# Kernel tuning notes

Measured on AMD Instinct MI355X. Metric: run time of the kernel, lower is better.

## Reference

```python
import jax, jax.numpy as jnp
import numpy as np

N = 8  # nodes per sample (hardcoded in preprocess)
NEG_SLOPE = 0.2
BIG_NEG = -1e30


def _mlp3(x, w1, b1, w2, b2, w3, b3):
    h = jax.nn.relu(x @ w1 + b1)
    h = jax.nn.relu(h @ w2 + b2)
    return h @ w3 + b3


def _gabriel(p):
    # p: [B,N,3] (vis_latent). Returns symmetric boolean adjacency [B,N,N]
    # (no self loops) and pairwise distances [B,N,N].
    mid = (p[:, :, None, :] + p[:, None, :, :]) * 0.5          # [B,N,N,3]
    r2 = jnp.sum((p[:, :, None, :] - mid) ** 2, axis=-1)       # [B,N,N]
    # d2[b,i,j,k] = ||p[b,k] - mid[b,i,j]||^2
    d2 = jnp.sum((p[:, None, None, :, :] - mid[:, :, :, None, :]) ** 2, axis=-1)  # [B,N,N,N]
    eye = jnp.eye(N, dtype=bool)
    kmask = (~eye[:, None, :]) & (~eye[None, :, :])            # [N,N,N] k != i, k != j
    viol = jnp.any(kmask[None] & (d2 < r2[..., None]), axis=-1)
    adj = (~viol) & (~eye)[None]                               # [B,N,N]
    dist = jnp.sqrt(jnp.sum((p[:, :, None, :] - p[:, None, :, :]) ** 2, axis=-1) + 1e-30)
    return adj, dist


def _gatv2(x, mask, eattr, wl, bl, wr, br, we, att, bias):
    # Dense masked GATv2 (PyG semantics, heads=1).
    # x: [B,N,F]; mask: [B,N,N] bool (row i = target, col j = source);
    # eattr: [B,N,N,1] edge feature.
    xl = x @ wl + bl                                            # source transform [B,N,C]
    xr = x @ wr + br                                            # target transform [B,N,C]
    ee = eattr @ we                                             # [B,N,N,C]
    h = xr[:, :, None, :] + xl[:, None, :, :] + ee              # [B,N,N,C]
    h = jnp.where(h >= 0, h, NEG_SLOPE * h)                     # leaky_relu
    e = jnp.einsum('bijc,c->bij', h, att)
    e = jnp.where(mask, e, BIG_NEG)
    alpha = jax.nn.softmax(e, axis=-1) * mask                   # rows always contain self loop
    return jnp.einsum('bij,bjc->bic', alpha, xl) + bias


def _forward(x, enc_w1, enc_b1, enc_w2, enc_b2, enc_w3, enc_b3,
             g1_wl, g1_bl, g1_wr, g1_br, g1_we, g1_att, g1_bias,
             g2_wl, g2_bl, g2_wr, g2_br, g2_we, g2_att, g2_bias,
             skip_w, skip_b, dec_w1, dec_b1, dec_w2, dec_b2, dec_w3, dec_b3):
    B = x.shape[0]
    # preprocess: [agent_type=0, index, value]
    idx = jnp.broadcast_to(jnp.arange(N, dtype=x.dtype), (B, N))
    xp = jnp.stack([jnp.zeros_like(x), idx, x], axis=-1)        # [B,N,3]

    latent = _mlp3(xp, enc_w1, enc_b1, enc_w2, enc_b2, enc_w3, enc_b3)  # [B,N,3]
    vis = latent - jnp.mean(latent, axis=1, keepdims=True)
    std = jnp.std(vis, axis=1, ddof=1) + 1e-8                   # torch.std is unbiased
    vis = vis / std[:, None, :]

    adj, dist = _gabriel(vis)                                   # [B,N,N] bool / float
    eye = jnp.eye(N, dtype=bool)[None]
    mask = adj | eye                                            # add self loops
    n_edges = jnp.sum(adj, axis=(1, 2)).astype(x.dtype)
    mean_attr = jnp.sum(dist * adj, axis=(1, 2)) / jnp.maximum(n_edges, 1.0)
    eattr = jnp.where(eye, mean_attr[:, None, None], dist)[..., None]  # [B,N,N,1]

    h1 = jax.nn.relu(_gatv2(latent, mask, eattr, g1_wl, g1_bl, g1_wr, g1_br, g1_we, g1_att, g1_bias))
    h2 = _gatv2(h1, mask, eattr, g2_wl, g2_bl, g2_wr, g2_br, g2_we, g2_att, g2_bias)
    combined = h2 + latent @ skip_w + skip_b
    rec = _mlp3(combined, dec_w1, dec_b1, dec_w2, dec_b2, dec_w3, dec_b3)
    return xp, rec, vis, adj


def setup_inputs() -> dict:
    key = jax.random.key(0)
    ks = iter(jax.random.split(key, 32))
    B, H, L, F = 16384, 64, 3, 3

    def rn(shape, scale):
        return (jax.random.normal(next(ks), shape, dtype=jnp.float32) * scale)

    inp = {
        'x': jax.random.normal(next(ks), (B, N), dtype=jnp.float32),
        'enc_w1': rn((F, H), (1.0 / F) ** 0.5), 'enc_b1': jnp.zeros((H,), jnp.float32),
        'enc_w2': rn((H, H), (1.0 / H) ** 0.5), 'enc_b2': jnp.zeros((H,), jnp.float32),
        'enc_w3': rn((H, L), (1.0 / H) ** 0.5), 'enc_b3': jnp.zeros((L,), jnp.float32),
        'g1_wl': rn((L, H), (1.0 / L) ** 0.5), 'g1_bl': jnp.zeros((H,), jnp.float32),
        'g1_wr': rn((L, H), (1.0 / L) ** 0.5), 'g1_br': jnp.zeros((H,), jnp.float32),
        'g1_we': rn((1, H), 1.0), 'g1_att': rn((H,), (1.0 / H) ** 0.5),
        'g1_bias': jnp.zeros((H,), jnp.float32),
        'g2_wl': rn((H, L), (1.0 / H) ** 0.5), 'g2_bl': jnp.zeros((L,), jnp.float32),
        'g2_wr': rn((H, L), (1.0 / H) ** 0.5), 'g2_br': jnp.zeros((L,), jnp.float32),
        'g2_we': rn((1, L), 1.0), 'g2_att': rn((L,), (1.0 / L) ** 0.5),
        'g2_bias': jnp.zeros((L,), jnp.float32),
        'skip_w': rn((L, L), (1.0 / L) ** 0.5), 'skip_b': jnp.zeros((L,), jnp.float32),
        'dec_w1': rn((L, H), (1.0 / L) ** 0.5), 'dec_b1': jnp.zeros((H,), jnp.float32),
        'dec_w2': rn((H, H), (1.0 / H) ** 0.5), 'dec_b2': jnp.zeros((H,), jnp.float32),
        'dec_w3': rn((H, F), (1.0 / H) ** 0.5), 'dec_b3': jnp.zeros((F,), jnp.float32),
    }
    return inp


def reference(x, enc_w1, enc_b1, enc_w2, enc_b2, enc_w3, enc_b3,
              g1_wl, g1_bl, g1_wr, g1_br, g1_we, g1_att, g1_bias,
              g2_wl, g2_bl, g2_wr, g2_br, g2_we, g2_att, g2_bias,
              skip_w, skip_b, dec_w1, dec_b1, dec_w2, dec_b2, dec_w3, dec_b3):
    return _forward(x, enc_w1, enc_b1, enc_w2, enc_b2, enc_w3, enc_b3,
                    g1_wl, g1_bl, g1_wr, g1_br, g1_we, g1_att, g1_bias,
                    g2_wl, g2_bl, g2_wr, g2_br, g2_we, g2_att, g2_bias,
                    skip_w, skip_b, dec_w1, dec_b1, dec_w2, dec_b2, dec_w3, dec_b3)
```

## Files before the change

kernel.cpp:

```cpp
#include <hip/hip_runtime.h>
#include <math.h>


#define WFENCE() asm volatile("s_waitcnt lgkmcnt(0)" ::: "memory")

struct alignas(16) WaveScratch {
  union Big {
    double d[8][68];
    float  f[2][8][68];
  } big;
  float  alphaS[64];
  float  latSf[24];
  float  xl2S[24];
  float  xr2S[24];
  float  combS[24];
  double latSd[24];
  double visSd[24];
};

__global__ __launch_bounds__(256)
void gae_fused(const float* __restrict__ x,
               const float* __restrict__ enc_w1, const float* __restrict__ enc_b1,
               const float* __restrict__ enc_w2, const float* __restrict__ enc_b2,
               const float* __restrict__ enc_w3, const float* __restrict__ enc_b3,
               const float* __restrict__ g1_wl, const float* __restrict__ g1_bl,
               const float* __restrict__ g1_wr, const float* __restrict__ g1_br,
               const float* __restrict__ g1_we, const float* __restrict__ g1_att,
               const float* __restrict__ g1_bias,
               const float* __restrict__ g2_wl, const float* __restrict__ g2_bl,
               const float* __restrict__ g2_wr, const float* __restrict__ g2_br,
               const float* __restrict__ g2_we, const float* __restrict__ g2_att,
               const float* __restrict__ g2_bias,
               const float* __restrict__ skip_w, const float* __restrict__ skip_b,
               const float* __restrict__ dec_w1, const float* __restrict__ dec_b1,
               const float* __restrict__ dec_w2, const float* __restrict__ dec_b2,
               const float* __restrict__ dec_w3, const float* __restrict__ dec_b3,
               float* __restrict__ out, int B)
{
  __shared__ WaveScratch ws4[4];
  __shared__ __align__(16) float s_w3e[192];
  __shared__ __align__(16) float s_w3d[192];
  __shared__ __align__(16) float s_g2wl[192];
  __shared__ __align__(16) float s_g2wr[192];
  __shared__ __align__(16) float s_we1[64];
  __shared__ __align__(16) float s_att1[64];
  __shared__ float s_skw[9], s_skb[3], s_b3e[3], s_b3d[3];
  __shared__ float s_g2bl[3], s_g2br[3], s_g2we[3], s_g2att[3], s_g2bias[3];

  const int tid  = threadIdx.x;
  const int wid  = tid >> 6;
  const int lane = tid & 63;

  if (tid < 192) { s_w3e[tid] = enc_w3[tid]; s_w3d[tid] = dec_w3[tid];
                   s_g2wl[tid] = g2_wl[tid]; s_g2wr[tid] = g2_wr[tid]; }
  if (tid < 64)  { s_we1[tid] = g1_we[tid];  s_att1[tid] = g1_att[tid]; }
  if (tid < 9)   s_skw[tid] = skip_w[tid];
  if (tid < 3)   { s_skb[tid] = skip_b[tid]; s_b3e[tid] = enc_b3[tid]; s_b3d[tid] = dec_b3[tid];
                   s_g2bl[tid] = g2_bl[tid]; s_g2br[tid] = g2_br[tid]; s_g2we[tid] = g2_we[tid];
                   s_g2att[tid] = g2_att[tid]; s_g2bias[tid] = g2_bias[tid]; }

  const int s = blockIdx.x * 4 + wid;
  const bool active = (s < B);
  const int sc = active ? s : 0;
  WaveScratch& W = ws4[wid];

  const double ew1n = (double)enc_w1[64 + lane];
  const double ew1x = (double)enc_w1[128 + lane];
  const double eb1d = (double)enc_b1[lane];
  const double eb2d = (double)enc_b2[lane];
  const float wl0 = g1_wl[lane], wl1 = g1_wl[64 + lane], wl2 = g1_wl[128 + lane], blc = g1_bl[lane];
  const float wr0 = g1_wr[lane], wr1 = g1_wr[64 + lane], wr2 = g1_wr[128 + lane], brc = g1_br[lane];
  const float g1bias_c = g1_bias[lane];
  const float dwc0 = dec_w1[lane], dwc1 = dec_w1[64 + lane], dwc2 = dec_w1[128 + lane];
  const float db1c = dec_b1[lane], db2c = dec_b2[lane];

  __syncthreads();

  const float* xb = x + (size_t)sc * 8;
  if (active && lane < 24) {
    const int r = lane, n = r / 3, l = r - n * 3;
    float v = (l == 0) ? 0.0f : ((l == 1) ? (float)n : xb[n]);
    out[(size_t)s * 24 + r] = v;
  }
  #pragma unroll
  for (int n = 0; n < 8; ++n) {
    double v = (double)n * ew1n + (double)xb[n] * ew1x + eb1d;
    W.big.d[n][lane] = v > 0.0 ? v : 0.0;
  }
  WFENCE();

  double acc2[8];
  #pragma unroll
  for (int n = 0; n < 8; ++n) acc2[n] = eb2d;
  #pragma unroll
  for (int ch = 0; ch < 4; ++ch) {
    double wcd[16];
    #pragma unroll
    for (int t = 0; t < 16; ++t) wcd[t] = (double)enc_w2[(ch * 16 + t) * 64 + lane];
    #pragma unroll
    for (int t2 = 0; t2 < 8; ++t2) {
      #pragma unroll
      for (int n = 0; n < 8; ++n) {
        const double2 hv = *(const double2*)&W.big.d[n][ch * 16 + t2 * 2];
        acc2[n] = fma(hv.x, wcd[t2 * 2], acc2[n]);
        acc2[n] = fma(hv.y, wcd[t2 * 2 + 1], acc2[n]);
      }
    }
  }
  WFENCE();
  #pragma unroll
  for (int n = 0; n < 8; ++n) W.big.d[n][lane] = acc2[n] > 0.0 ? acc2[n] : 0.0;
  WFENCE();

  {
    const int r24 = lane & 31, g = lane >> 5;
    double a = 0.0;
    if (r24 < 24) {
      const int n = r24 / 3, l = r24 - n * 3;
      a = g ? 0.0 : (double)s_b3e[l];
      const int k0 = g * 32;
      #pragma unroll 8
      for (int k = k0; k < k0 + 32; ++k) a = fma(W.big.d[n][k], (double)s_w3e[k * 3 + l], a);
    }
    const double b = __shfl_xor(a, 32);
    if (lane < 24) {
      const double tot = a + b;
      W.latSd[lane] = tot;
      W.latSf[lane] = (float)tot;
    }
  }
  WFENCE();

  if (lane < 24) {
    const int r = lane, l = r % 3;
    double s1 = 0.0;
    #pragma unroll
    for (int q = 0; q < 8; ++q) s1 += W.latSd[q * 3 + l];
    const double m = s1 * 0.125;
    double s2 = 0.0;
    #pragma unroll
    for (int q = 0; q < 8; ++q) s2 += (W.latSd[q * 3 + l] - m);
    const double m2 = s2 * 0.125;
    double s3 = 0.0;
    #pragma unroll
    for (int q = 0; q < 8; ++q) { double dv = W.latSd[q * 3 + l] - m - m2; s3 += dv * dv; }
    const double stdv = sqrt(s3 / 7.0) + 1e-8;
    const double visv = (W.latSd[r] - m) / stdv;
    W.visSd[r] = visv;
    if (active) out[(size_t)B * 48 + (size_t)s * 24 + r] = (float)visv;
  }
  WFENCE();

  const int gi = lane >> 3, gj = lane & 7;
  const double pi0 = W.visSd[gi * 3], pi1 = W.visSd[gi * 3 + 1], pi2 = W.visSd[gi * 3 + 2];
  const double pj0 = W.visSd[gj * 3], pj1 = W.visSd[gj * 3 + 1], pj2 = W.visSd[gj * 3 + 2];
  const double mid0 = (pi0 + pj0) * 0.5, mid1 = (pi1 + pj1) * 0.5, mid2 = (pi2 + pj2) * 0.5;
  const double dr0 = pi0 - mid0, dr1 = pi1 - mid1, dr2 = pi2 - mid2;
  const double r2 = dr0 * dr0 + dr1 * dr1 + dr2 * dr2;
  bool viol = false;
  #pragma unroll
  for (int k = 0; k < 8; ++k) {
    const double a0 = W.visSd[k * 3] - mid0;
    const double a1 = W.visSd[k * 3 + 1] - mid1;
    const double a2 = W.visSd[k * 3 + 2] - mid2;
    const double d2 = a0 * a0 + a1 * a1 + a2 * a2;
    viol = viol || ((k != gi) && (k != gj) && (d2 < r2));
  }
  const double dd0 = pi0 - pj0, dd1 = pi1 - pj1, dd2 = pi2 - pj2;
  const double distd = sqrt(dd0 * dd0 + dd1 * dd1 + dd2 * dd2 + 1e-30);
  const bool adjb  = (!viol) && (gi != gj);
  const bool maskb = adjb || (gi == gj);
  const float adjf = adjb ? 1.0f : 0.0f;
  if (active) out[(size_t)B * 72 + (size_t)s * 64 + lane] = adjf;
  const float distf = (float)distd;
  float ne = adjf, sd = adjb ? distf : 0.0f;
  #pragma unroll
  for (int d = 1; d < 64; d <<= 1) { ne += __shfl_xor(ne, d); sd += __shfl_xor(sd, d); }
  const float mean_attr = sd / fmaxf(ne, 1.0f);
  const float eat = (gi == gj) ? mean_attr : distf;

  float xlr[8], xrr[8];
  #pragma unroll
  for (int n = 0; n < 8; ++n) {
    const float a0 = W.latSf[n * 3], a1 = W.latSf[n * 3 + 1], a2 = W.latSf[n * 3 + 2];
    xlr[n] = fmaf(a2, wl2, fmaf(a1, wl1, fmaf(a0, wl0, blc)));
    xrr[n] = fmaf(a2, wr2, fmaf(a1, wr1, fmaf(a0, wr0, brc)));
    W.big.f[0][n][lane] = xlr[n];
    W.big.f[1][n][lane] = xrr[n];
  }
  WFENCE();

  float ev = 0.0f;
  #pragma unroll
  for (int c4 = 0; c4 < 16; ++c4) {
    const float4 xlv = *(const float4*)&W.big.f[0][gj][c4 * 4];
    const float4 xrv = *(const float4*)&W.big.f[1][gi][c4 * 4];
    const float4 wev = *(const float4*)&s_we1[c4 * 4];
    const float4 atv = *(const float4*)&s_att1[c4 * 4];
    float h;
    h = fmaf(eat, wev.x, xrv.x + xlv.x); ev = fmaf(fmaxf(h, 0.f) + 0.2f * fminf(h, 0.f), atv.x, ev);
    h = fmaf(eat, wev.y, xrv.y + xlv.y); ev = fmaf(fmaxf(h, 0.f) + 0.2f * fminf(h, 0.f), atv.y, ev);
    h = fmaf(eat, wev.z, xrv.z + xlv.z); ev = fmaf(fmaxf(h, 0.f) + 0.2f * fminf(h, 0.f), atv.z, ev);
    h = fmaf(eat, wev.w, xrv.w + xlv.w); ev = fmaf(fmaxf(h, 0.f) + 0.2f * fminf(h, 0.f), atv.w, ev);
  }
  {
    float em = maskb ? ev : -1e30f;
    float mx = em;
    mx = fmaxf(mx, __shfl_xor(mx, 1)); mx = fmaxf(mx, __shfl_xor(mx, 2)); mx = fmaxf(mx, __shfl_xor(mx, 4));
    float p = __expf(em - mx);
    float ssum = p;
    ssum += __shfl_xor(ssum, 1); ssum += __shfl_xor(ssum, 2); ssum += __shfl_xor(ssum, 4);
    W.alphaS[lane] = (p / ssum) * (maskb ? 1.0f : 0.0f);
  }
  WFENCE();

  float hg[8];
  #pragma unroll
  for (int i = 0; i < 8; ++i) {
    const float4 q0 = *(const float4*)&W.alphaS[i * 8];
    const float4 q1 = *(const float4*)&W.alphaS[i * 8 + 4];
    float a = g1bias_c;
    a = fmaf(q0.x, xlr[0], a); a = fmaf(q0.y, xlr[1], a);
    a = fmaf(q0.z, xlr[2], a); a = fmaf(q0.w, xlr[3], a);
    a = fmaf(q1.x, xlr[4], a); a = fmaf(q1.y, xlr[5], a);
    a = fmaf(q1.z, xlr[6], a); a = fmaf(q1.w, xlr[7], a);
    hg[i] = fmaxf(a, 0.0f);
  }
  WFENCE();
  #pragma unroll
  for (int i = 0; i < 8; ++i) W.big.f[0][i][lane] = hg[i];
  WFENCE();

  if (lane < 48) {
    const int g = lane / 24, r = lane - g * 24, n = r / 3, l = r - n * 3;
    const float* wsel = g ? s_g2wr : s_g2wl;
    float a = g ? s_g2br[l] : s_g2bl[l];
    #pragma unroll 8
    for (int k = 0; k < 64; ++k) a = fmaf(W.big.f[0][n][k], wsel[k * 3 + l], a);
    if (g) W.xr2S[r] = a; else W.xl2S[r] = a;
  }
  WFENCE();

  float e2 = 0.0f;
  #pragma unroll
  for (int l = 0; l < 3; ++l) {
    const float hh = fmaf(eat, s_g2we[l], W.xr2S[gi * 3 + l] + W.xl2S[gj * 3 + l]);
    e2 = fmaf(fmaxf(hh, 0.f) + 0.2f * fminf(hh, 0.f), s_g2att[l], e2);
  }
  {
    float em = maskb ? e2 : -1e30f;
    float mx = em;
    mx = fmaxf(mx, __shfl_xor(mx, 1)); mx = fmaxf(mx, __shfl_xor(mx, 2)); mx = fmaxf(mx, __shfl_xor(mx, 4));
    float p = __expf(em - mx);
    float ssum = p;
    ssum += __shfl_xor(ssum, 1); ssum += __shfl_xor(ssum, 2); ssum += __shfl_xor(ssum, 4);
    W.alphaS[lane] = (p / ssum) * (maskb ? 1.0f : 0.0f);
  }
  WFENCE();

  if (lane < 24) {
    const int r = lane, n = r / 3, l = r - n * 3;
    float a = s_g2bias[l];
    #pragma unroll
    for (int j = 0; j < 8; ++j) a = fmaf(W.alphaS[n * 8 + j], W.xl2S[j * 3 + l], a);
    const float cb = a + W.latSf[n * 3] * s_skw[l] + W.latSf[n * 3 + 1] * s_skw[3 + l]
                       + W.latSf[n * 3 + 2] * s_skw[6 + l] + s_skb[l];
    W.combS[r] = cb;
  }
  WFENCE();

  #pragma unroll
  for (int n = 0; n < 8; ++n) {
    const float c0 = W.combS[n * 3], c1 = W.combS[n * 3 + 1], c2 = W.combS[n * 3 + 2];
    const float d1 = fmaf(c2, dwc2, fmaf(c1, dwc1, fmaf(c0, dwc0, db1c)));
    W.big.f[0][n][lane] = fmaxf(d1, 0.0f);
  }
  WFENCE();

  float accf[8];
  #pragma unroll
  for (int n = 0; n < 8; ++n) accf[n] = db2c;
  #pragma unroll
  for (int ch = 0; ch < 2; ++ch) {
    float wc[32];
    #pragma unroll
    for (int t = 0; t < 32; ++t) wc[t] = dec_w2[(ch * 32 + t) * 64 + lane];
    #pragma unroll
    for (int t4 = 0; t4 < 8; ++t4) {
      #pragma unroll
      for (int n = 0; n < 8; ++n) {
        const float4 hv = *(const float4*)&W.big.f[0][n][ch * 32 + t4 * 4];
        accf[n] = fmaf(hv.x, wc[t4 * 4], accf[n]);
        accf[n] = fmaf(hv.y, wc[t4 * 4 + 1], accf[n]);
        accf[n] = fmaf(hv.z, wc[t4 * 4 + 2], accf[n]);
        accf[n] = fmaf(hv.w, wc[t4 * 4 + 3], accf[n]);
      }
    }
  }
  WFENCE();
  #pragma unroll
  for (int n = 0; n < 8; ++n) W.big.f[1][n][lane] = fmaxf(accf[n], 0.0f);
  WFENCE();

  {
    const int r24 = lane & 31, g = lane >> 5;
    float a = 0.0f;
    if (r24 < 24) {
      const int n = r24 / 3, l = r24 - n * 3;
      a = g ? 0.0f : s_b3d[l];
      const int k0 = g * 32;
      #pragma unroll 8
      for (int k = k0; k < k0 + 32; ++k) a = fmaf(W.big.f[1][n][k], s_w3d[k * 3 + l], a);
    }
    const float b = __shfl_xor(a, 32);
    if (active && lane < 24) {
      out[(size_t)B * 24 + (size_t)s * 24 + lane] = a + b;
    }
  }
}

extern "C" void kernel_launch(void* const* d_in, const int* in_sizes, int n_in,
                              void* d_out, int out_size, void* d_ws, size_t ws_size,
                              hipStream_t stream) {
  const int B = in_sizes[0] / 8;
  const float* x       = (const float*)d_in[0];
  const float* enc_w1  = (const float*)d_in[1];
  const float* enc_b1  = (const float*)d_in[2];
  const float* enc_w2  = (const float*)d_in[3];
  const float* enc_b2  = (const float*)d_in[4];
  const float* enc_w3  = (const float*)d_in[5];
  const float* enc_b3  = (const float*)d_in[6];
  const float* g1_wl   = (const float*)d_in[7];
  const float* g1_bl   = (const float*)d_in[8];
  const float* g1_wr   = (const float*)d_in[9];
  const float* g1_br   = (const float*)d_in[10];
  const float* g1_we   = (const float*)d_in[11];
  const float* g1_att  = (const float*)d_in[12];
  const float* g1_bias = (const float*)d_in[13];
  const float* g2_wl   = (const float*)d_in[14];
  const float* g2_bl   = (const float*)d_in[15];
  const float* g2_wr   = (const float*)d_in[16];
  const float* g2_br   = (const float*)d_in[17];
  const float* g2_we   = (const float*)d_in[18];
  const float* g2_att  = (const float*)d_in[19];
  const float* g2_bias = (const float*)d_in[20];
  const float* skip_w  = (const float*)d_in[21];
  const float* skip_b  = (const float*)d_in[22];
  const float* dec_w1  = (const float*)d_in[23];
  const float* dec_b1  = (const float*)d_in[24];
  const float* dec_w2  = (const float*)d_in[25];
  const float* dec_b2  = (const float*)d_in[26];
  const float* dec_w3  = (const float*)d_in[27];
  const float* dec_b3  = (const float*)d_in[28];
  float* out = (float*)d_out;

  const int nblk = (B + 3) / 4;
  gae_fused<<<nblk, 256, 0, stream>>>(x,
      enc_w1, enc_b1, enc_w2, enc_b2, enc_w3, enc_b3,
      g1_wl, g1_bl, g1_wr, g1_br, g1_we, g1_att, g1_bias,
      g2_wl, g2_bl, g2_wr, g2_br, g2_we, g2_att, g2_bias,
      skip_w, skip_b, dec_w1, dec_b1, dec_w2, dec_b2, dec_w3, dec_b3,
      out, B);
}
```

Baseline: 95.40 us.

## Shrink LDS scratch, cap registers for 8 waves, split accumulators in dot products

Cuts per-wave LDS by overlaying scratch buffers inside the big union and dropping the shared copies of small weight matrices, which are now read straight from global/L2. Launch bounds now request 8 blocks per CU, and the weight-chunk register arrays are halved so more waves fit. Long serial FMA chains are split into four partial accumulators for more ILP, and the mean/std stage uses wave shuffles instead of an LDS round trip. The cost is more global loads of the small weights and possible register spilling under the tighter bound.

```diff
diff --git a/kernel.cpp b/kernel.cpp
--- a/kernel.cpp
+++ b/kernel.cpp
@@ -5,20 +5,15 @@
 #define WFENCE() asm volatile("s_waitcnt lgkmcnt(0)" ::: "memory")
 
 struct alignas(16) WaveScratch {
-  union Big {
+  union {
     double d[8][68];
-    float  f[2][8][68];
+    float  f[16][68];
   } big;
-  float  alphaS[64];
-  float  latSf[24];
-  float  xl2S[24];
-  float  xr2S[24];
-  float  combS[24];
-  double latSd[24];
-  double visSd[24];
+  float extra[112];
+  float latSf[24];
 };
 
-__global__ __launch_bounds__(256)
+__global__ __launch_bounds__(256, 8)
 void gae_fused(const float* __restrict__ x,
                const float* __restrict__ enc_w1, const float* __restrict__ enc_b1,
                const float* __restrict__ enc_w2, const float* __restrict__ enc_b2,
@@ -38,10 +33,6 @@
                float* __restrict__ out, int B)
 {
   __shared__ WaveScratch ws4[4];
-  __shared__ __align__(16) float s_w3e[192];
-  __shared__ __align__(16) float s_w3d[192];
-  __shared__ __align__(16) float s_g2wl[192];
-  __shared__ __align__(16) float s_g2wr[192];
   __shared__ __align__(16) float s_we1[64];
   __shared__ __align__(16) float s_att1[64];
   __shared__ float s_skw[9], s_skb[3], s_b3e[3], s_b3d[3];
@@ -51,8 +42,6 @@
   const int wid  = tid >> 6;
   const int lane = tid & 63;
 
-  if (tid < 192) { s_w3e[tid] = enc_w3[tid]; s_w3d[tid] = dec_w3[tid];
-                   s_g2wl[tid] = g2_wl[tid]; s_g2wr[tid] = g2_wr[tid]; }
   if (tid < 64)  { s_we1[tid] = g1_we[tid];  s_att1[tid] = g1_att[tid]; }
   if (tid < 9)   s_skw[tid] = skip_w[tid];
   if (tid < 3)   { s_skb[tid] = skip_b[tid]; s_b3e[tid] = enc_b3[tid]; s_b3d[tid] = dec_b3[tid];
@@ -93,15 +82,15 @@
   #pragma unroll
   for (int n = 0; n < 8; ++n) acc2[n] = eb2d;
   #pragma unroll
-  for (int ch = 0; ch < 4; ++ch) {
-    double wcd[16];
-    #pragma unroll
-    for (int t = 0; t < 16; ++t) wcd[t] = (double)enc_w2[(ch * 16 + t) * 64 + lane];
-    #pragma unroll
-    for (int t2 = 0; t2 < 8; ++t2) {
+  for (int ch = 0; ch < 8; ++ch) {
+    double wcd[8];
+    #pragma unroll
+    for (int t = 0; t < 8; ++t) wcd[t] = (double)enc_w2[(ch * 8 + t) * 64 + lane];
+    #pragma unroll
+    for (int t2 = 0; t2 < 4; ++t2) {
       #pragma unroll
       for (int n = 0; n < 8; ++n) {
-        const double2 hv = *(const double2*)&W.big.d[n][ch * 16 + t2 * 2];
+        const double2 hv = *(const double2*)&W.big.d[n][ch * 8 + t2 * 2];
         acc2[n] = fma(hv.x, wcd[t2 * 2], acc2[n]);
         acc2[n] = fma(hv.y, wcd[t2 * 2 + 1], acc2[n]);
       }
@@ -112,57 +101,61 @@
   for (int n = 0; n < 8; ++n) W.big.d[n][lane] = acc2[n] > 0.0 ? acc2[n] : 0.0;
   WFENCE();
 
+  double totd;
   {
     const int r24 = lane & 31, g = lane >> 5;
-    double a = 0.0;
-    if (r24 < 24) {
-      const int n = r24 / 3, l = r24 - n * 3;
-      a = g ? 0.0 : (double)s_b3e[l];
-      const int k0 = g * 32;
-      #pragma unroll 8
-      for (int k = k0; k < k0 + 32; ++k) a = fma(W.big.d[n][k], (double)s_w3e[k * 3 + l], a);
-    }
-    const double b = __shfl_xor(a, 32);
+    const int n = (r24 < 24) ? r24 / 3 : 0;
+    const int l = (r24 < 24) ? r24 % 3 : 0;
+    const int k0 = g * 32;
+    double p0 = 0.0, p1 = 0.0, p2 = 0.0, p3 = 0.0;
+    #pragma unroll
+    for (int kk = 0; kk < 8; ++kk) {
+      p0 = fma(W.big.d[n][k0 + kk],      (double)enc_w3[(k0 + kk) * 3 + l],      p0);
+      p1 = fma(W.big.d[n][k0 + 8 + kk],  (double)enc_w3[(k0 + 8 + kk) * 3 + l],  p1);
+      p2 = fma(W.big.d[n][k0 + 16 + kk], (double)enc_w3[(k0 + 16 + kk) * 3 + l], p2);
+      p3 = fma(W.big.d[n][k0 + 24 + kk], (double)enc_w3[(k0 + 24 + kk) * 3 + l], p3);
+    }
+    double a = ((p0 + p1) + (p2 + p3)) + (g ? 0.0 : (double)s_b3e[l]);
+    totd = a + __shfl_xor(a, 32);
+    if (lane < 24) W.latSf[lane] = (float)totd;
+  }
+
+  double* const visSd = (double*)&W.big.f[15][0];
+  {
+    const int l = lane % 3;
+    double v[8];
+    #pragma unroll
+    for (int q = 0; q < 8; ++q) v[q] = __shfl(totd, q * 3 + l);
     if (lane < 24) {
-      const double tot = a + b;
-      W.latSd[lane] = tot;
-      W.latSf[lane] = (float)tot;
-    }
-  }
-  WFENCE();
-
-  if (lane < 24) {
-    const int r = lane, l = r % 3;
-    double s1 = 0.0;
-    #pragma unroll
-    for (int q = 0; q < 8; ++q) s1 += W.latSd[q * 3 + l];
-    const double m = s1 * 0.125;
-    double s2 = 0.0;
-    #pragma unroll
-    for (int q = 0; q < 8; ++q) s2 += (W.latSd[q * 3 + l] - m);
-    const double m2 = s2 * 0.125;
-    double s3 = 0.0;
-    #pragma unroll
-    for (int q = 0; q < 8; ++q) { double dv = W.latSd[q * 3 + l] - m - m2; s3 += dv * dv; }
-    const double stdv = sqrt(s3 / 7.0) + 1e-8;
-    const double visv = (W.latSd[r] - m) / stdv;
-    W.visSd[r] = visv;
-    if (active) out[(size_t)B * 48 + (size_t)s * 24 + r] = (float)visv;
+      const double s1 = ((v[0] + v[1]) + (v[2] + v[3])) + ((v[4] + v[5]) + (v[6] + v[7]));
+      const double m = s1 * 0.125;
+      double s2 = 0.0;
+      #pragma unroll
+      for (int q = 0; q < 8; ++q) s2 += (v[q] - m);
+      const double m2 = s2 * 0.125;
+      double s3 = 0.0;
+      #pragma unroll
+      for (int q = 0; q < 8; ++q) { const double dv = v[q] - m - m2; s3 += dv * dv; }
+      const double stdv = sqrt(s3 / 7.0) + 1e-8;
+      const double visv = (totd - m) / stdv;
+      visSd[lane] = visv;
+      if (active) out[(size_t)B * 48 + (size_t)s * 24 + lane] = (float)visv;
+    }
   }
   WFENCE();
 
   const int gi = lane >> 3, gj = lane & 7;
-  const double pi0 = W.visSd[gi * 3], pi1 = W.visSd[gi * 3 + 1], pi2 = W.visSd[gi * 3 + 2];
-  const double pj0 = W.visSd[gj * 3], pj1 = W.visSd[gj * 3 + 1], pj2 = W.visSd[gj * 3 + 2];
+  const double pi0 = visSd[gi * 3], pi1 = visSd[gi * 3 + 1], pi2 = visSd[gi * 3 + 2];
+  const double pj0 = visSd[gj * 3], pj1 = visSd[gj * 3 + 1], pj2 = visSd[gj * 3 + 2];
   const double mid0 = (pi0 + pj0) * 0.5, mid1 = (pi1 + pj1) * 0.5, mid2 = (pi2 + pj2) * 0.5;
   const double dr0 = pi0 - mid0, dr1 = pi1 - mid1, dr2 = pi2 - mid2;
   const double r2 = dr0 * dr0 + dr1 * dr1 + dr2 * dr2;
   bool viol = false;
   #pragma unroll
   for (int k = 0; k < 8; ++k) {
-    const double a0 = W.visSd[k * 3] - mid0;
-    const double a1 = W.visSd[k * 3 + 1] - mid1;
-    const double a2 = W.visSd[k * 3 + 2] - mid2;
+    const double a0 = visSd[k * 3] - mid0;
+    const double a1 = visSd[k * 3 + 1] - mid1;
+    const double a2 = visSd[k * 3 + 2] - mid2;
     const double d2 = a0 * a0 + a1 * a1 + a2 * a2;
     viol = viol || ((k != gi) && (k != gj) && (d2 < r2));
   }
@@ -185,40 +178,41 @@
     const float a0 = W.latSf[n * 3], a1 = W.latSf[n * 3 + 1], a2 = W.latSf[n * 3 + 2];
     xlr[n] = fmaf(a2, wl2, fmaf(a1, wl1, fmaf(a0, wl0, blc)));
     xrr[n] = fmaf(a2, wr2, fmaf(a1, wr1, fmaf(a0, wr0, brc)));
-    W.big.f[0][n][lane] = xlr[n];
-    W.big.f[1][n][lane] = xrr[n];
-  }
-  WFENCE();
-
-  float ev = 0.0f;
-  #pragma unroll
-  for (int c4 = 0; c4 < 16; ++c4) {
-    const float4 xlv = *(const float4*)&W.big.f[0][gj][c4 * 4];
-    const float4 xrv = *(const float4*)&W.big.f[1][gi][c4 * 4];
-    const float4 wev = *(const float4*)&s_we1[c4 * 4];
-    const float4 atv = *(const float4*)&s_att1[c4 * 4];
-    float h;
-    h = fmaf(eat, wev.x, xrv.x + xlv.x); ev = fmaf(fmaxf(h, 0.f) + 0.2f * fminf(h, 0.f), atv.x, ev);
-    h = fmaf(eat, wev.y, xrv.y + xlv.y); ev = fmaf(fmaxf(h, 0.f) + 0.2f * fminf(h, 0.f), atv.y, ev);
-    h = fmaf(eat, wev.z, xrv.z + xlv.z); ev = fmaf(fmaxf(h, 0.f) + 0.2f * fminf(h, 0.f), atv.z, ev);
-    h = fmaf(eat, wev.w, xrv.w + xlv.w); ev = fmaf(fmaxf(h, 0.f) + 0.2f * fminf(h, 0.f), atv.w, ev);
-  }
-  {
+    W.big.f[n][lane]     = xlr[n];
+    W.big.f[8 + n][lane] = xrr[n];
+  }
+  WFENCE();
+
+  {
+    float ev0 = 0.0f, ev1 = 0.0f, ev2 = 0.0f, ev3 = 0.0f;
+    #pragma unroll
+    for (int c4 = 0; c4 < 16; ++c4) {
+      const float4 xlv = *(const float4*)&W.big.f[gj][c4 * 4];
+      const float4 xrv = *(const float4*)&W.big.f[8 + gi][c4 * 4];
+      const float4 wev = *(const float4*)&s_we1[c4 * 4];
+      const float4 atv = *(const float4*)&s_att1[c4 * 4];
+      float h;
+      h = fmaf(eat, wev.x, xrv.x + xlv.x); ev0 = fmaf(fmaxf(h, 0.f) + 0.2f * fminf(h, 0.f), atv.x, ev0);
+      h = fmaf(eat, wev.y, xrv.y + xlv.y); ev1 = fmaf(fmaxf(h, 0.f) + 0.2f * fminf(h, 0.f), atv.y, ev1);
+      h = fmaf(eat, wev.z, xrv.z + xlv.z); ev2 = fmaf(fmaxf(h, 0.f) + 0.2f * fminf(h, 0.f), atv.z, ev2);
+      h = fmaf(eat, wev.w, xrv.w + xlv.w); ev3 = fmaf(fmaxf(h, 0.f) + 0.2f * fminf(h, 0.f), atv.w, ev3);
+    }
+    const float ev = (ev0 + ev1) + (ev2 + ev3);
     float em = maskb ? ev : -1e30f;
     float mx = em;
     mx = fmaxf(mx, __shfl_xor(mx, 1)); mx = fmaxf(mx, __shfl_xor(mx, 2)); mx = fmaxf(mx, __shfl_xor(mx, 4));
     float p = __expf(em - mx);
     float ssum = p;
     ssum += __shfl_xor(ssum, 1); ssum += __shfl_xor(ssum, 2); ssum += __shfl_xor(ssum, 4);
-    W.alphaS[lane] = (p / ssum) * (maskb ? 1.0f : 0.0f);
+    W.extra[lane] = (p / ssum) * (maskb ? 1.0f : 0.0f);
   }
   WFENCE();
 
   float hg[8];
   #pragma unroll
   for (int i = 0; i < 8; ++i) {
-    const float4 q0 = *(const float4*)&W.alphaS[i * 8];
-    const float4 q1 = *(const float4*)&W.alphaS[i * 8 + 4];
+    const float4 q0 = *(const float4*)&W.extra[i * 8];
+    const float4 q1 = *(const float4*)&W.extra[i * 8 + 4];
     float a = g1bias_c;
     a = fmaf(q0.x, xlr[0], a); a = fmaf(q0.y, xlr[1], a);
     a = fmaf(q0.z, xlr[2], a); a = fmaf(q0.w, xlr[3], a);
@@ -228,33 +222,39 @@
   }
   WFENCE();
   #pragma unroll
-  for (int i = 0; i < 8; ++i) W.big.f[0][i][lane] = hg[i];
+  for (int i = 0; i < 8; ++i) W.big.f[i][lane] = hg[i];
   WFENCE();
 
   if (lane < 48) {
     const int g = lane / 24, r = lane - g * 24, n = r / 3, l = r - n * 3;
-    const float* wsel = g ? s_g2wr : s_g2wl;
-    float a = g ? s_g2br[l] : s_g2bl[l];
-    #pragma unroll 8
-    for (int k = 0; k < 64; ++k) a = fmaf(W.big.f[0][n][k], wsel[k * 3 + l], a);
-    if (g) W.xr2S[r] = a; else W.xl2S[r] = a;
-  }
-  WFENCE();
-
-  float e2 = 0.0f;
-  #pragma unroll
-  for (int l = 0; l < 3; ++l) {
-    const float hh = fmaf(eat, s_g2we[l], W.xr2S[gi * 3 + l] + W.xl2S[gj * 3 + l]);
-    e2 = fmaf(fmaxf(hh, 0.f) + 0.2f * fminf(hh, 0.f), s_g2att[l], e2);
-  }
-  {
+    const float* __restrict__ wsel = g ? g2_wr : g2_wl;
+    float p0 = 0.f, p1 = 0.f, p2 = 0.f, p3 = 0.f;
+    #pragma unroll
+    for (int kk = 0; kk < 16; ++kk) {
+      p0 = fmaf(W.big.f[n][kk],      wsel[(kk) * 3 + l],      p0);
+      p1 = fmaf(W.big.f[n][16 + kk], wsel[(16 + kk) * 3 + l], p1);
+      p2 = fmaf(W.big.f[n][32 + kk], wsel[(32 + kk) * 3 + l], p2);
+      p3 = fmaf(W.big.f[n][48 + kk], wsel[(48 + kk) * 3 + l], p3);
+    }
+    const float a = ((p0 + p1) + (p2 + p3)) + (g ? s_g2br[l] : s_g2bl[l]);
+    W.extra[64 + g * 24 + r] = a;
+  }
+  WFENCE();
+
+  {
+    float e2 = 0.0f;
+    #pragma unroll
+    for (int l = 0; l < 3; ++l) {
+      const float hh = fmaf(eat, s_g2we[l], W.extra[88 + gi * 3 + l] + W.extra[64 + gj * 3 + l]);
+      e2 = fmaf(fmaxf(hh, 0.f) + 0.2f * fminf(hh, 0.f), s_g2att[l], e2);
+    }
     float em = maskb ? e2 : -1e30f;
     float mx = em;
     mx = fmaxf(mx, __shfl_xor(mx, 1)); mx = fmaxf(mx, __shfl_xor(mx, 2)); mx = fmaxf(mx, __shfl_xor(mx, 4));
     float p = __expf(em - mx);
     float ssum = p;
     ssum += __shfl_xor(ssum, 1); ssum += __shfl_xor(ssum, 2); ssum += __shfl_xor(ssum, 4);
-    W.alphaS[lane] = (p / ssum) * (maskb ? 1.0f : 0.0f);
+    W.extra[lane] = (p / ssum) * (maskb ? 1.0f : 0.0f);
   }
   WFENCE();
 
@@ -262,18 +262,21 @@
     const int r = lane, n = r / 3, l = r - n * 3;
     float a = s_g2bias[l];
     #pragma unroll
-    for (int j = 0; j < 8; ++j) a = fmaf(W.alphaS[n * 8 + j], W.xl2S[j * 3 + l], a);
+    for (int j = 0; j < 8; ++j) a = fmaf(W.extra[n * 8 + j], W.extra[64 + j * 3 + l], a);
     const float cb = a + W.latSf[n * 3] * s_skw[l] + W.latSf[n * 3 + 1] * s_skw[3 + l]
                        + W.latSf[n * 3 + 2] * s_skw[6 + l] + s_skb[l];
-    W.combS[r] = cb;
+    W.big.f[r >> 2][64 + (r & 3)] = cb;
   }
   WFENCE();
 
   #pragma unroll
   for (int n = 0; n < 8; ++n) {
-    const float c0 = W.combS[n * 3], c1 = W.combS[n * 3 + 1], c2 = W.combS[n * 3 + 2];
+    const int r0 = n * 3, r1 = n * 3 + 1, r2i = n * 3 + 2;
+    const float c0 = W.big.f[r0 >> 2][64 + (r0 & 3)];
+    const float c1 = W.big.f[r1 >> 2][64 + (r1 & 3)];
+    const float c2 = W.big.f[r2i >> 2][64 + (r2i & 3)];
     const float d1 = fmaf(c2, dwc2, fmaf(c1, dwc1, fmaf(c0, dwc0, db1c)));
-    W.big.f[0][n][lane] = fmaxf(d1, 0.0f);
+    W.big.f[n][lane] = fmaxf(d1, 0.0f);
   }
   WFENCE();
 
@@ -281,15 +284,15 @@
   #pragma unroll
   for (int n = 0; n < 8; ++n) accf[n] = db2c;
   #pragma unroll
-  for (int ch = 0; ch < 2; ++ch) {
-    float wc[32];
-    #pragma unroll
-    for (int t = 0; t < 32; ++t) wc[t] = dec_w2[(ch * 32 + t) * 64 + lane];
-    #pragma unroll
-    for (int t4 = 0; t4 < 8; ++t4) {
+  for (int ch = 0; ch < 4; ++ch) {
+    float wc[16];
+    #pragma unroll
+    for (int t = 0; t < 16; ++t) wc[t] = dec_w2[(ch * 16 + t) * 64 + lane];
+    #pragma unroll
+    for (int t4 = 0; t4 < 4; ++t4) {
       #pragma unroll
       for (int n = 0; n < 8; ++n) {
-        const float4 hv = *(const float4*)&W.big.f[0][n][ch * 32 + t4 * 4];
+        const float4 hv = *(const float4*)&W.big.f[n][ch * 16 + t4 * 4];
         accf[n] = fmaf(hv.x, wc[t4 * 4], accf[n]);
         accf[n] = fmaf(hv.y, wc[t4 * 4 + 1], accf[n]);
         accf[n] = fmaf(hv.z, wc[t4 * 4 + 2], accf[n]);
@@ -299,19 +302,23 @@
   }
   WFENCE();
   #pragma unroll
-  for (int n = 0; n < 8; ++n) W.big.f[1][n][lane] = fmaxf(accf[n], 0.0f);
+  for (int n = 0; n < 8; ++n) W.big.f[8 + n][lane] = fmaxf(accf[n], 0.0f);
   WFENCE();
 
   {
     const int r24 = lane & 31, g = lane >> 5;
-    float a = 0.0f;
-    if (r24 < 24) {
-      const int n = r24 / 3, l = r24 - n * 3;
-      a = g ? 0.0f : s_b3d[l];
-      const int k0 = g * 32;
-      #pragma unroll 8
-      for (int k = k0; k < k0 + 32; ++k) a = fmaf(W.big.f[1][n][k], s_w3d[k * 3 + l], a);
-    }
+    const int n = (r24 < 24) ? r24 / 3 : 0;
+    const int l = (r24 < 24) ? r24 % 3 : 0;
+    const int k0 = g * 32;
+    float p0 = 0.f, p1 = 0.f, p2 = 0.f, p3 = 0.f;
+    #pragma unroll
+    for (int kk = 0; kk < 8; ++kk) {
+      p0 = fmaf(W.big.f[8 + n][k0 + kk],      dec_w3[(k0 + kk) * 3 + l],      p0);
+      p1 = fmaf(W.big.f[8 + n][k0 + 8 + kk],  dec_w3[(k0 + 8 + kk) * 3 + l],  p1);
+      p2 = fmaf(W.big.f[8 + n][k0 + 16 + kk], dec_w3[(k0 + 16 + kk) * 3 + l], p2);
+      p3 = fmaf(W.big.f[8 + n][k0 + 24 + kk], dec_w3[(k0 + 24 + kk) * 3 + l], p3);
+    }
+    float a = ((p0 + p1) + (p2 + p3)) + (g ? 0.f : s_b3d[l]);
     const float b = __shfl_xor(a, 32);
     if (active && lane < 24) {
       out[(size_t)B * 24 + (size_t)s * 24 + lane] = a + b;
```

After: 349.3 us. +266.1%, slower.
